# Kernel tuning notes

Hardware: AMD Instinct MI355X
Metric: run time of the kernel (lower is better)

The kernel has to match this reference:

```python
import jax, jax.numpy as jnp
import numpy as np

N_LEVELS = 16  # 3**16 = 43_046_721


def setup_inputs() -> dict:
    key = jax.random.key(0)
    k1, k2 = jax.random.split(key)
    f = jax.random.normal(k1, (3 ** N_LEVELS,), dtype=jnp.float32)
    # torch.rand -> uniform [0, 1)
    Phi_P = jax.random.uniform(k2, (N_LEVELS, 3, 3), dtype=jnp.float32)
    return {"f": f, "Phi_P": Phi_P}


def reference(f, Phi_P):
    N = Phi_P.shape[0]
    # Row-orthonormalize each 3x3 block: QR of Phi_P^T, then take Q^T
    Q, _ = jnp.linalg.qr(jnp.swapaxes(Phi_P, -2, -1))  # batched reduced QR
    Phi = jnp.swapaxes(Q, -2, -1)  # [N, 3, 3], orthonormal rows

    # Recursive Haar-style butterfly. At level i, f has length 3**(N-i).
    # Detail coefficients (rows j=1,2) land in slots [3**(N-i-1), 3**(N-i));
    # the row-0 (average) branch recurses. Build segments and concatenate
    # in reverse to avoid scatter into a preallocated buffer.
    segs = []
    for i in range(N):
        fm = f.reshape(-1, 3)            # [3**(N-i-1), 3]
        d1 = fm @ Phi[i, 1, :]           # detail j=1
        d2 = fm @ Phi[i, 2, :]           # detail j=2
        segs.append(jnp.concatenate([d1, d2]))
        f = fm @ Phi[i, 0, :]            # average branch, length /3
    # f now has length 1; its single entry is f_hat[0]
    f_hat = jnp.concatenate([f[:1]] + segs[::-1])
    return f_hat
```

## Files before the change

kernel.cpp:

```cpp
#include <hip/hip_runtime.h>

#define TPB 256

__device__ __forceinline__ float sgpr(float x) {
    return __int_as_float(__builtin_amdgcn_readfirstlane(__float_as_int(x)));
}

__device__ __forceinline__ float gather3(float v0, float v1, float v2, int e) {
    int s = e & 63;
    float t0 = __shfl(v0, s);
    float t1 = __shfl(v1, s);
    float t2 = __shfl(v2, s);
    int r = e >> 6;
    return r == 0 ? t0 : (r == 1 ? t1 : t2);
}

__device__ __forceinline__ void qr3(const float* __restrict__ M, float* __restrict__ P) {
    float A[3][3];
#pragma unroll
    for (int r = 0; r < 3; ++r)
#pragma unroll
        for (int c = 0; c < 3; ++c)
            A[r][c] = M[c * 3 + r];

    float V[3][3], tau[3];
#pragma unroll
    for (int k = 0; k < 3; ++k) {
        float alpha = A[k][k];
        float xn2 = 0.f;
#pragma unroll
        for (int r = k + 1; r < 3; ++r) xn2 += A[r][k] * A[r][k];
        float t = 0.f;
        float v[3] = {0.f, 0.f, 0.f};
        v[k] = 1.f;
        if (xn2 > 0.f) {
            float beta = -copysignf(sqrtf(alpha * alpha + xn2), alpha);
            t = (beta - alpha) / beta;
            float inv = 1.f / (alpha - beta);
#pragma unroll
            for (int r = k + 1; r < 3; ++r) v[r] = A[r][k] * inv;
#pragma unroll
            for (int c = 0; c < 3; ++c) {
                if (c < k) continue;
                float w = 0.f;
#pragma unroll
                for (int r = 0; r < 3; ++r) if (r >= k) w += v[r] * A[r][c];
                w *= t;
#pragma unroll
                for (int r = 0; r < 3; ++r) if (r >= k) A[r][c] -= w * v[r];
            }
        }
        tau[k] = t;
#pragma unroll
        for (int r = 0; r < 3; ++r) V[k][r] = v[r];
    }
    float Q[3][3] = {{1.f, 0.f, 0.f}, {0.f, 1.f, 0.f}, {0.f, 0.f, 1.f}};
#pragma unroll
    for (int k = 2; k >= 0; --k) {
#pragma unroll
        for (int c = 0; c < 3; ++c) {
            float w = 0.f;
#pragma unroll
            for (int r = 0; r < 3; ++r) w += V[k][r] * Q[r][c];
            w *= tau[k];
#pragma unroll
            for (int r = 0; r < 3; ++r) Q[r][c] -= w * V[k][r];
        }
    }
#pragma unroll
    for (int r = 0; r < 3; ++r)
#pragma unroll
        for (int c = 0; c < 3; ++c)
            P[r * 3 + c] = Q[c][r];
}

__global__ __launch_bounds__(TPB) void fused3_kernel(
        const float* __restrict__ in, float* __restrict__ out,
        float* __restrict__ avg_out, const float* __restrict__ PhiP,
        int lvl, int m2) {
    const int lane = threadIdx.x & 63;
    const int w    = threadIdx.x >> 6;
    const long N0 = 9L * m2, N1 = 3L * m2, N2 = m2;
    const long M0 = 9L * m2, M1 = 3L * m2, M2 = m2;
    const long T0 = 2304L * blockIdx.x + 576L * w;
    const long T1 = T0 / 3;
    const long T2 = T0 / 9;

    const bool interior = (T0 + 576 <= N0);

    float v[9][3];
    if (interior) {
        const float* base = in + 3 * T0;
#pragma unroll
        for (int r = 0; r < 9; ++r)
#pragma unroll
            for (int c = 0; c < 3; ++c)
                v[r][c] = base[192L * r + 64 * c + lane];
    }

    float P[27];
    qr3(PhiP + 9L * lvl,       P + 0);
    qr3(PhiP + 9L * (lvl + 1), P + 9);
    qr3(PhiP + 9L * (lvl + 2), P + 18);
#pragma unroll
    for (int j = 0; j < 27; ++j) P[j] = sgpr(P[j]);

    float a[9];
    if (interior) {
#pragma unroll
        for (int g = 0; g < 9; ++g) {
            float x = gather3(v[g][0], v[g][1], v[g][2], 3 * lane + 0);
            float y = gather3(v[g][0], v[g][1], v[g][2], 3 * lane + 1);
            float z = gather3(v[g][0], v[g][1], v[g][2], 3 * lane + 2);
            float av = x * P[0] + y * P[1] + z * P[2];
            float d1 = x * P[3] + y * P[4] + z * P[5];
            float d2 = x * P[6] + y * P[7] + z * P[8];
            long t = T0 + 64L * g + lane;
            __builtin_nontemporal_store(d1, out + M0 + t);
            __builtin_nontemporal_store(d2, out + 2 * M0 + t);
            a[g] = av;
        }
    } else {
#pragma unroll
        for (int g = 0; g < 9; ++g) {
            long t = T0 + 64L * g + lane;
            float x = 0.f, y = 0.f, z = 0.f;
            if (t < N0) {
                const float* p = in + 3 * t;
                x = p[0]; y = p[1]; z = p[2];
            }
            float av = x * P[0] + y * P[1] + z * P[2];
            float d1 = x * P[3] + y * P[4] + z * P[5];
            float d2 = x * P[6] + y * P[7] + z * P[8];
            if (t < N0) {
                __builtin_nontemporal_store(d1, out + M0 + t);
                __builtin_nontemporal_store(d2, out + 2 * M0 + t);
            }
            a[g] = av;
        }
    }

    float b[3];
#pragma unroll
    for (int h = 0; h < 3; ++h) {
        float x = gather3(a[3 * h], a[3 * h + 1], a[3 * h + 2], 3 * lane + 0);
        float y = gather3(a[3 * h], a[3 * h + 1], a[3 * h + 2], 3 * lane + 1);
        float z = gather3(a[3 * h], a[3 * h + 1], a[3 * h + 2], 3 * lane + 2);
        float bv = x * P[9]  + y * P[10] + z * P[11];
        float d1 = x * P[12] + y * P[13] + z * P[14];
        float d2 = x * P[15] + y * P[16] + z * P[17];
        long j = T1 + 64L * h + lane;
        if (j < N1) {
            __builtin_nontemporal_store(d1, out + M1 + j);
            __builtin_nontemporal_store(d2, out + 2 * M1 + j);
        }
        b[h] = bv;
    }

    {
        float x = gather3(b[0], b[1], b[2], 3 * lane + 0);
        float y = gather3(b[0], b[1], b[2], 3 * lane + 1);
        float z = gather3(b[0], b[1], b[2], 3 * lane + 2);
        float cv = x * P[18] + y * P[19] + z * P[20];
        float d1 = x * P[21] + y * P[22] + z * P[23];
        float d2 = x * P[24] + y * P[25] + z * P[26];
        long u = T2 + lane;
        if (u < N2) {
            __builtin_nontemporal_store(d1, out + M2 + u);
            __builtin_nontemporal_store(d2, out + 2 * M2 + u);
            avg_out[u] = cv;
        }
    }
}

#define TTPB 1024
__global__ __launch_bounds__(TTPB) void tail_kernel(
        const float* __restrict__ in, float* __restrict__ out,
        const float* __restrict__ PhiP) {
    __shared__ float s0[2187];
    __shared__ float s1[729];
    __shared__ float sPhi[63];
    const int lt = threadIdx.x;

    for (int i = lt; i < 2187; i += TTPB) s0[i] = in[i];
    if (lt < 7) {
        float P[9];
        qr3(PhiP + 9L * (9 + lt), P);
#pragma unroll
        for (int j = 0; j < 9; ++j) sPhi[lt * 9 + j] = P[j];
    }
    __syncthreads();

    float* cur = s0;
    float* nxt = s1;
    int len = 2187;
#pragma unroll
    for (int L = 0; L < 7; ++L) {
        int m = len / 3;
        float p0 = sPhi[L * 9 + 0], p1 = sPhi[L * 9 + 1], p2 = sPhi[L * 9 + 2];
        float q0 = sPhi[L * 9 + 3], q1 = sPhi[L * 9 + 4], q2 = sPhi[L * 9 + 5];
        float r0 = sPhi[L * 9 + 6], r1 = sPhi[L * 9 + 7], r2 = sPhi[L * 9 + 8];
        for (int t = lt; t < m; t += TTPB) {
            float x = cur[3 * t], y = cur[3 * t + 1], z = cur[3 * t + 2];
            out[m + t]     = x * q0 + y * q1 + z * q2;
            out[2 * m + t] = x * r0 + y * r1 + z * r2;
            nxt[t]         = x * p0 + y * p1 + z * p2;
        }
        asm volatile("s_waitcnt lgkmcnt(0)" ::: "memory");
        __builtin_amdgcn_s_barrier();
        float* tmp = cur; cur = nxt; nxt = tmp;
        len = m;
    }
    if (lt == 0) out[0] = cur[0];
}

extern "C" void kernel_launch(void* const* d_in, const int* in_sizes, int n_in,
                              void* d_out, int out_size, void* d_ws, size_t ws_size,
                              hipStream_t stream) {
    const float* f    = (const float*)d_in[0];
    const float* PhiP = (const float*)d_in[1];
    float* out = (float*)d_out;
    float* ws  = (float*)d_ws;

    float* bufA = ws;
    float* bufB = bufA + 1594323;
    float* bufC = bufB + 59049;

    const int m2_0 = 1594323;
    fused3_kernel<<<(m2_0 + TPB - 1) / TPB, TPB, 0, stream>>>(f, out, bufA, PhiP, 0, m2_0);

    const int m2_1 = 59049;
    fused3_kernel<<<(m2_1 + TPB - 1) / TPB, TPB, 0, stream>>>(bufA, out, bufB, PhiP, 3, m2_1);

    const int m2_2 = 2187;
    fused3_kernel<<<(m2_2 + TPB - 1) / TPB, TPB, 0, stream>>>(bufB, out, bufC, PhiP, 6, m2_2);

    tail_kernel<<<1, TTPB, 0, stream>>>(bufC, out, PhiP);
}
```

Measured before the change: 85.55 us.

## Stage fused three-level butterfly through LDS instead of wave shuffles

```diff
diff --git a/kernel.cpp b/kernel.cpp
--- a/kernel.cpp
+++ b/kernel.cpp
@@ -1,18 +1,15 @@
 #include <hip/hip_runtime.h>
 
 #define TPB 256
+
+__device__ __forceinline__ void block_sync_lds() {
+    asm volatile("s_waitcnt lgkmcnt(0)" ::: "memory");
+    __builtin_amdgcn_s_barrier();
+    asm volatile("" ::: "memory");
+}
 
 __device__ __forceinline__ float sgpr(float x) {
     return __int_as_float(__builtin_amdgcn_readfirstlane(__float_as_int(x)));
-}
-
-__device__ __forceinline__ float gather3(float v0, float v1, float v2, int e) {
-    int s = e & 63;
-    float t0 = __shfl(v0, s);
-    float t1 = __shfl(v1, s);
-    float t2 = __shfl(v2, s);
-    int r = e >> 6;
-    return r == 0 ? t0 : (r == 1 ? t1 : t2);
 }
 
 __device__ __forceinline__ void qr3(const float* __restrict__ M, float* __restrict__ P) {
@@ -78,24 +75,21 @@
         const float* __restrict__ in, float* __restrict__ out,
         float* __restrict__ avg_out, const float* __restrict__ PhiP,
         int lvl, int m2) {
-    const int lane = threadIdx.x & 63;
-    const int w    = threadIdx.x >> 6;
-    const long N0 = 9L * m2, N1 = 3L * m2, N2 = m2;
+    __shared__ float s[6912];
+    const int  t = threadIdx.x;
+    const long b = blockIdx.x;
+    const long nF = 27L * m2;
+    const long fBase = 6912L * b;
     const long M0 = 9L * m2, M1 = 3L * m2, M2 = m2;
-    const long T0 = 2304L * blockIdx.x + 576L * w;
-    const long T1 = T0 / 3;
-    const long T2 = T0 / 9;
-
-    const bool interior = (T0 + 576 <= N0);
-
-    float v[9][3];
-    if (interior) {
-        const float* base = in + 3 * T0;
-#pragma unroll
-        for (int r = 0; r < 9; ++r)
-#pragma unroll
-            for (int c = 0; c < 3; ++c)
-                v[r][c] = base[192L * r + 64 * c + lane];
+
+    const bool fullLoad = (fBase + 6912 <= nF);
+
+    float4 v[7];
+    if (fullLoad) {
+        const float4* p4 = reinterpret_cast<const float4*>(in + fBase);
+#pragma unroll
+        for (int r = 0; r < 6; ++r) v[r] = p4[256 * r + t];
+        if (t < 192) v[6] = p4[1536 + t];
     }
 
     float P[27];
@@ -105,70 +99,78 @@
 #pragma unroll
     for (int j = 0; j < 27; ++j) P[j] = sgpr(P[j]);
 
+    if (fullLoad) {
+#pragma unroll
+        for (int r = 0; r < 6; ++r)
+            *reinterpret_cast<float4*>(&s[4 * (256 * r + t)]) = v[r];
+        if (t < 192)
+            *reinterpret_cast<float4*>(&s[4 * (1536 + t)]) = v[6];
+    } else {
+        const long rem = nF - fBase;
+        for (int i = t; i < 6912; i += TPB) s[i] = (i < rem) ? in[fBase + i] : 0.f;
+    }
+    block_sync_lds();
+
+    float f[27];
+#pragma unroll
+    for (int j = 0; j < 27; ++j) f[j] = s[27 * t + j];
+    block_sync_lds();
+
     float a[9];
-    if (interior) {
-#pragma unroll
-        for (int g = 0; g < 9; ++g) {
-            float x = gather3(v[g][0], v[g][1], v[g][2], 3 * lane + 0);
-            float y = gather3(v[g][0], v[g][1], v[g][2], 3 * lane + 1);
-            float z = gather3(v[g][0], v[g][1], v[g][2], 3 * lane + 2);
-            float av = x * P[0] + y * P[1] + z * P[2];
-            float d1 = x * P[3] + y * P[4] + z * P[5];
-            float d2 = x * P[6] + y * P[7] + z * P[8];
-            long t = T0 + 64L * g + lane;
-            __builtin_nontemporal_store(d1, out + M0 + t);
-            __builtin_nontemporal_store(d2, out + 2 * M0 + t);
-            a[g] = av;
-        }
+#pragma unroll
+    for (int g = 0; g < 9; ++g) {
+        float x = f[3 * g], y = f[3 * g + 1], z = f[3 * g + 2];
+        a[g] = x * P[0] + y * P[1] + z * P[2];
+        s[9 * t + g]        = x * P[3] + y * P[4] + z * P[5];
+        s[2304 + 9 * t + g] = x * P[6] + y * P[7] + z * P[8];
+    }
+    float bb[3];
+#pragma unroll
+    for (int h = 0; h < 3; ++h) {
+        float x = a[3 * h], y = a[3 * h + 1], z = a[3 * h + 2];
+        bb[h] = x * P[9] + y * P[10] + z * P[11];
+        s[4608 + 3 * t + h] = x * P[12] + y * P[13] + z * P[14];
+        s[5376 + 3 * t + h] = x * P[15] + y * P[16] + z * P[17];
+    }
+    float c;
+    {
+        float x = bb[0], y = bb[1], z = bb[2];
+        c = x * P[18] + y * P[19] + z * P[20];
+        s[6144 + t] = x * P[21] + y * P[22] + z * P[23];
+        s[6400 + t] = x * P[24] + y * P[25] + z * P[26];
+    }
+    block_sync_lds();
+
+    const bool fullStore = (2304L * (b + 1) <= M0);
+    if (fullStore) {
+        const long g0 = 2304 * b, g1 = 768 * b, g2 = 256 * b;
+#pragma unroll
+        for (int r = 0; r < 9; ++r) out[M0 + g0 + 256 * r + t]     = s[256 * r + t];
+#pragma unroll
+        for (int r = 0; r < 9; ++r) out[2 * M0 + g0 + 256 * r + t] = s[2304 + 256 * r + t];
+#pragma unroll
+        for (int r = 0; r < 3; ++r) out[M1 + g1 + 256 * r + t]     = s[4608 + 256 * r + t];
+#pragma unroll
+        for (int r = 0; r < 3; ++r) out[2 * M1 + g1 + 256 * r + t] = s[5376 + 256 * r + t];
+        out[M2 + g2 + t]     = s[6144 + t];
+        out[2 * M2 + g2 + t] = s[6400 + t];
+        avg_out[g2 + t]      = c;
     } else {
 #pragma unroll
-        for (int g = 0; g < 9; ++g) {
-            long t = T0 + 64L * g + lane;
-            float x = 0.f, y = 0.f, z = 0.f;
-            if (t < N0) {
-                const float* p = in + 3 * t;
-                x = p[0]; y = p[1]; z = p[2];
-            }
-            float av = x * P[0] + y * P[1] + z * P[2];
-            float d1 = x * P[3] + y * P[4] + z * P[5];
-            float d2 = x * P[6] + y * P[7] + z * P[8];
-            if (t < N0) {
-                __builtin_nontemporal_store(d1, out + M0 + t);
-                __builtin_nontemporal_store(d2, out + 2 * M0 + t);
-            }
-            a[g] = av;
-        }
-    }
-
-    float b[3];
-#pragma unroll
-    for (int h = 0; h < 3; ++h) {
-        float x = gather3(a[3 * h], a[3 * h + 1], a[3 * h + 2], 3 * lane + 0);
-        float y = gather3(a[3 * h], a[3 * h + 1], a[3 * h + 2], 3 * lane + 1);
-        float z = gather3(a[3 * h], a[3 * h + 1], a[3 * h + 2], 3 * lane + 2);
-        float bv = x * P[9]  + y * P[10] + z * P[11];
-        float d1 = x * P[12] + y * P[13] + z * P[14];
-        float d2 = x * P[15] + y * P[16] + z * P[17];
-        long j = T1 + 64L * h + lane;
-        if (j < N1) {
-            __builtin_nontemporal_store(d1, out + M1 + j);
-            __builtin_nontemporal_store(d2, out + 2 * M1 + j);
-        }
-        b[h] = bv;
-    }
-
-    {
-        float x = gather3(b[0], b[1], b[2], 3 * lane + 0);
-        float y = gather3(b[0], b[1], b[2], 3 * lane + 1);
-        float z = gather3(b[0], b[1], b[2], 3 * lane + 2);
-        float cv = x * P[18] + y * P[19] + z * P[20];
-        float d1 = x * P[21] + y * P[22] + z * P[23];
-        float d2 = x * P[24] + y * P[25] + z * P[26];
-        long u = T2 + lane;
-        if (u < N2) {
-            __builtin_nontemporal_store(d1, out + M2 + u);
-            __builtin_nontemporal_store(d2, out + 2 * M2 + u);
-            avg_out[u] = cv;
+        for (int r = 0; r < 9; ++r) {
+            long i = 256 * r + t, g = 2304 * b + i;
+            if (g < M0) { out[M0 + g] = s[i]; out[2 * M0 + g] = s[2304 + i]; }
+        }
+#pragma unroll
+        for (int r = 0; r < 3; ++r) {
+            long i = 256 * r + t, g = 768 * b + i;
+            if (g < M1) { out[M1 + g] = s[4608 + i]; out[2 * M1 + g] = s[5376 + i]; }
+        }
+        long g = 256 * b + t;
+        if (g < M2) {
+            out[M2 + g]     = s[6144 + t];
+            out[2 * M2 + g] = s[6400 + t];
+            avg_out[g]      = c;
         }
     }
 }
@@ -206,8 +208,7 @@
             out[2 * m + t] = x * r0 + y * r1 + z * r2;
             nxt[t]         = x * p0 + y * p1 + z * p2;
         }
-        asm volatile("s_waitcnt lgkmcnt(0)" ::: "memory");
-        __builtin_amdgcn_s_barrier();
+        block_sync_lds();
         float* tmp = cur; cur = nxt; nxt = tmp;
         len = m;
     }
```

Measured after the change: 138.7 us. 62.2% more time.
